# Kernel tuning notes

Hardware: AMD Instinct MI355X
Metric: run time of the kernel (lower is better)

The kernel has to match this reference:

```python
import jax, jax.numpy as jnp
import numpy as np

SPATIAL_SIZE = (1.0, 1.0)
SPATIAL_ORIGIN = (0.0, 0.0)
GRID = (64, 64)
N_FEATURES = 128


def setup_inputs() -> dict:
    key = jax.random.key(0)
    k1, k2 = jax.random.split(key)
    positions = jax.random.uniform(k1, (8, 256, 256, 2), dtype=jnp.float32)
    embeddings = jax.random.normal(k2, (GRID[0], GRID[1], N_FEATURES), dtype=jnp.float32)
    return {"positions": positions, "embeddings": embeddings}


def reference(positions, embeddings):
    Gx, Gy, _ = embeddings.shape
    x = (positions[..., 0] - SPATIAL_ORIGIN[0]) / SPATIAL_SIZE[0] * Gx
    y = (positions[..., 1] - SPATIAL_ORIGIN[1]) / SPATIAL_SIZE[1] * Gy
    x0 = jnp.floor(x).astype(jnp.int32)
    y0 = jnp.floor(y).astype(jnp.int32)
    x1 = jnp.clip(x0 + 1, 0, Gx - 1)
    y1 = jnp.clip(y0 + 1, 0, Gy - 1)
    x0c = jnp.clip(x0, 0, Gx - 1)
    y0c = jnp.clip(y0, 0, Gy - 1)
    # four corner gathers: [b,h,w,F]
    fx0y0 = embeddings[x0c, y0c]
    fx0y1 = embeddings[x0c, y1]
    fx1y0 = embeddings[x1, y0c]
    fx1y1 = embeddings[x1, y1]
    dx = (x - x0.astype(x.dtype))[..., None]
    dy = (y - y0.astype(y.dtype))[..., None]
    fxy0 = fx0y0 * (1 - dx) + fx1y0 * dx
    fxy1 = fx0y1 * (1 - dx) + fx1y1 * dx
    return fxy0 * (1 - dy) + fxy1 * dy
```

## Files before the change

kernel.cpp:

```cpp
#include <hip/hip_runtime.h>

#define GX 64
#define GY 64
#define NF 128
#define NPOINTS (8 * 256 * 256)
#define C4 (NF / 4)
#define LPP 8
#define CPT (C4 / LPP)

typedef float v4f __attribute__((ext_vector_type(4)));

__device__ __forceinline__ v4f lerp2(const v4f a, const v4f b,
                                     const v4f cc, const v4f d,
                                     float omdx, float dx,
                                     float omdy, float dy) {
    v4f top = a * omdx + b * dx;
    v4f bot = cc * omdx + d * dx;
    return top * omdy + bot * dy;
}

__global__ __launch_bounds__(256) void bilerp2d_kernel(
    const float* __restrict__ pos,
    const float* __restrict__ emb,
    float* __restrict__ out)
{
    const v4f* __restrict__ e4 = reinterpret_cast<const v4f*>(emb);
    v4f* __restrict__ out4 = reinterpret_cast<v4f*>(out);
    const float2* __restrict__ pos2 = reinterpret_cast<const float2*>(pos);

    const unsigned int idx = blockIdx.x * blockDim.x + threadIdx.x;
    const unsigned int point = idx >> 3;
    const unsigned int c     = idx & (LPP - 1);

    const float2 p = pos2[point];

    const float xf = p.x * (float)GX;
    const float yf = p.y * (float)GY;
    const float fx0 = floorf(xf);
    const float fy0 = floorf(yf);
    const int x0 = (int)fx0;
    const int y0 = (int)fy0;
    const float dx = xf - fx0;
    const float dy = yf - fy0;

    const int x0c = min(max(x0, 0), GX - 1);
    const int y0c = min(max(y0, 0), GY - 1);
    const int x1  = min(max(x0 + 1, 0), GX - 1);
    const int y1  = min(max(y0 + 1, 0), GY - 1);

    const unsigned b00 = (unsigned)(x0c * GY + y0c) * C4 + c;
    const unsigned b10 = (unsigned)(x1  * GY + y0c) * C4 + c;
    const unsigned b01 = (unsigned)(x0c * GY + y1 ) * C4 + c;
    const unsigned b11 = (unsigned)(x1  * GY + y1 ) * C4 + c;

    v4f f00[CPT], f10[CPT], f01[CPT], f11[CPT];
#pragma unroll
    for (int k = 0; k < CPT; ++k) {
        f00[k] = e4[b00 + k * LPP];
        f10[k] = e4[b10 + k * LPP];
        f01[k] = e4[b01 + k * LPP];
        f11[k] = e4[b11 + k * LPP];
    }

    const float omdx = 1.0f - dx;
    const float omdy = 1.0f - dy;

    const unsigned obase = point * C4 + c;
#pragma unroll
    for (int k = 0; k < CPT; ++k) {
        const v4f r = lerp2(f00[k], f10[k], f01[k], f11[k], omdx, dx, omdy, dy);
        __builtin_nontemporal_store(r, &out4[obase + k * LPP]);
    }
}

extern "C" void kernel_launch(void* const* d_in, const int* in_sizes, int n_in,
                              void* d_out, int out_size, void* d_ws, size_t ws_size,
                              hipStream_t stream) {
    const float* positions  = (const float*)d_in[0];
    const float* embeddings = (const float*)d_in[1];
    float* out = (float*)d_out;

    const int block = 256;
    const int grid = (NPOINTS * LPP) / block;
    bilerp2d_kernel<<<grid, block, 0, stream>>>(positions, embeddings, out);
}
```

Measured before the change: 57.68 us.

## Bin points by grid cell via histogram, scan, scatter before bilinear gather

Adds a counting-sort pipeline (histogram, prefix scan, atomic scatter) that reorders point indices by grid cell so the main interpolation kernel processes spatially coherent points and gets better cache locality on embedding gathers. The direct kernel remains as a fallback when the workspace is too small. The preprocessing adds three extra kernels, a memset and atomics. Output writes become scattered by original point index, and with only a 2 MB embedding table that already fits in cache, the locality gain may be small compared with this added cost.

```diff
diff --git a/kernel.cpp b/kernel.cpp
--- a/kernel.cpp
+++ b/kernel.cpp
@@ -7,6 +7,7 @@
 #define C4 (NF / 4)
 #define LPP 8
 #define CPT (C4 / LPP)
+#define NBINS (GX * GY)
 
 typedef float v4f __attribute__((ext_vector_type(4)));
 
@@ -19,9 +20,72 @@
     return top * omdy + bot * dy;
 }
 
-__global__ __launch_bounds__(256) void bilerp2d_kernel(
+__device__ __forceinline__ int cell_of(float2 p) {
+    int x0 = (int)floorf(p.x * (float)GX);
+    int y0 = (int)floorf(p.y * (float)GY);
+    int xc = min(max(x0, 0), GX - 1);
+    int yc = min(max(y0, 0), GY - 1);
+    return xc * GY + yc;
+}
+
+
+__global__ __launch_bounds__(256) void hist_kernel(
+    const float2* __restrict__ pos2, unsigned int* __restrict__ hist)
+{
+    __shared__ unsigned int lh[NBINS];
+    for (int t = threadIdx.x; t < NBINS; t += 256) lh[t] = 0;
+    __syncthreads();
+    const unsigned int stride = gridDim.x * blockDim.x;
+    for (unsigned int i = blockIdx.x * blockDim.x + threadIdx.x;
+         i < NPOINTS; i += stride)
+        atomicAdd(&lh[cell_of(pos2[i])], 1u);
+    __syncthreads();
+    for (int t = threadIdx.x; t < NBINS; t += 256) {
+        unsigned int v = lh[t];
+        if (v) atomicAdd(&hist[t], v);
+    }
+}
+
+__global__ __launch_bounds__(256) void scan_kernel(
+    const unsigned int* __restrict__ hist, unsigned int* __restrict__ offs)
+{
+    __shared__ unsigned int sums[256];
+    unsigned int local[16];
+    const int base = threadIdx.x * 16;
+    unsigned int s = 0;
+#pragma unroll
+    for (int k = 0; k < 16; ++k) { local[k] = hist[base + k]; s += local[k]; }
+    sums[threadIdx.x] = s;
+    __syncthreads();
+    for (int d = 1; d < 256; d <<= 1) {
+        unsigned int v = (threadIdx.x >= (unsigned)d) ? sums[threadIdx.x - d] : 0u;
+        __syncthreads();
+        sums[threadIdx.x] += v;
+        __syncthreads();
+    }
+    unsigned int excl = sums[threadIdx.x] - s;
+#pragma unroll
+    for (int k = 0; k < 16; ++k) { offs[base + k] = excl; excl += local[k]; }
+}
+
+__global__ __launch_bounds__(256) void scatter_kernel(
+    const float2* __restrict__ pos2, unsigned int* __restrict__ offs,
+    unsigned int* __restrict__ binned)
+{
+    const unsigned int stride = gridDim.x * blockDim.x;
+    for (unsigned int i = blockIdx.x * blockDim.x + threadIdx.x;
+         i < NPOINTS; i += stride) {
+        int c = cell_of(pos2[i]);
+        unsigned int slot = atomicAdd(&offs[c], 1u);
+        binned[slot] = i;
+    }
+}
+
+
+__global__ __launch_bounds__(256) void bilerp2d_binned(
     const float* __restrict__ pos,
     const float* __restrict__ emb,
+    const unsigned int* __restrict__ binned,
     float* __restrict__ out)
 {
     const v4f* __restrict__ e4 = reinterpret_cast<const v4f*>(emb);
@@ -29,9 +93,10 @@
     const float2* __restrict__ pos2 = reinterpret_cast<const float2*>(pos);
 
     const unsigned int idx = blockIdx.x * blockDim.x + threadIdx.x;
-    const unsigned int point = idx >> 3;
-    const unsigned int c     = idx & (LPP - 1);
-
+    const unsigned int slot = idx >> 3;
+    const unsigned int c    = idx & (LPP - 1);
+
+    const unsigned int point = binned[slot];
     const float2 p = pos2[point];
 
     const float xf = p.x * (float)GX;
@@ -73,14 +138,82 @@
     }
 }
 
+
+__global__ __launch_bounds__(256) void bilerp2d_direct(
+    const float* __restrict__ pos,
+    const float* __restrict__ emb,
+    float* __restrict__ out)
+{
+    const v4f* __restrict__ e4 = reinterpret_cast<const v4f*>(emb);
+    v4f* __restrict__ out4 = reinterpret_cast<v4f*>(out);
+    const float2* __restrict__ pos2 = reinterpret_cast<const float2*>(pos);
+
+    const unsigned int idx = blockIdx.x * blockDim.x + threadIdx.x;
+    const unsigned int point = idx >> 3;
+    const unsigned int c     = idx & (LPP - 1);
+
+    const float2 p = pos2[point];
+    const float xf = p.x * (float)GX;
+    const float yf = p.y * (float)GY;
+    const float fx0 = floorf(xf);
+    const float fy0 = floorf(yf);
+    const int x0 = (int)fx0;
+    const int y0 = (int)fy0;
+    const float dx = xf - fx0;
+    const float dy = yf - fy0;
+
+    const int x0c = min(max(x0, 0), GX - 1);
+    const int y0c = min(max(y0, 0), GY - 1);
+    const int x1  = min(max(x0 + 1, 0), GX - 1);
+    const int y1  = min(max(y0 + 1, 0), GY - 1);
+
+    const unsigned b00 = (unsigned)(x0c * GY + y0c) * C4 + c;
+    const unsigned b10 = (unsigned)(x1  * GY + y0c) * C4 + c;
+    const unsigned b01 = (unsigned)(x0c * GY + y1 ) * C4 + c;
+    const unsigned b11 = (unsigned)(x1  * GY + y1 ) * C4 + c;
+
+    v4f f00[CPT], f10[CPT], f01[CPT], f11[CPT];
+#pragma unroll
+    for (int k = 0; k < CPT; ++k) {
+        f00[k] = e4[b00 + k * LPP];
+        f10[k] = e4[b10 + k * LPP];
+        f01[k] = e4[b01 + k * LPP];
+        f11[k] = e4[b11 + k * LPP];
+    }
+
+    const float omdx = 1.0f - dx;
+    const float omdy = 1.0f - dy;
+    const unsigned obase = point * C4 + c;
+#pragma unroll
+    for (int k = 0; k < CPT; ++k) {
+        const v4f r = lerp2(f00[k], f10[k], f01[k], f11[k], omdx, dx, omdy, dy);
+        __builtin_nontemporal_store(r, &out4[obase + k * LPP]);
+    }
+}
+
 extern "C" void kernel_launch(void* const* d_in, const int* in_sizes, int n_in,
                               void* d_out, int out_size, void* d_ws, size_t ws_size,
                               hipStream_t stream) {
     const float* positions  = (const float*)d_in[0];
     const float* embeddings = (const float*)d_in[1];
     float* out = (float*)d_out;
-
+    const float2* pos2 = (const float2*)positions;
+
+    const size_t need = (size_t)(2 * NBINS + NPOINTS) * sizeof(unsigned int);
     const int block = 256;
-    const int grid = (NPOINTS * LPP) / block;
-    bilerp2d_kernel<<<grid, block, 0, stream>>>(positions, embeddings, out);
-}
+    const int main_grid = (NPOINTS * LPP) / block;
+
+    if (ws_size >= need) {
+        unsigned int* hist   = (unsigned int*)d_ws;
+        unsigned int* offs   = hist + NBINS;
+        unsigned int* binned = offs + NBINS;
+
+        hipMemsetAsync(hist, 0, NBINS * sizeof(unsigned int), stream);
+        hist_kernel<<<256, block, 0, stream>>>(pos2, hist);
+        scan_kernel<<<1, block, 0, stream>>>(hist, offs);
+        scatter_kernel<<<512, block, 0, stream>>>(pos2, offs, binned);
+        bilerp2d_binned<<<main_grid, block, 0, stream>>>(positions, embeddings, binned, out);
+    } else {
+        bilerp2d_direct<<<main_grid, block, 0, stream>>>(positions, embeddings, out);
+    }
+}
```

Result: slower. 115.6 us (+100.3%).
